# Kernel tuning notes

Measured on AMD Instinct MI355X. Metric: run time of the kernel, lower is better.

The kernel has to match this reference:

```python
import math
import jax, jax.numpy as jnp
import numpy as np

NUM_HEADS = 8
K_CRITICAL = 0.05
K_SKIP = 0.10


def setup_inputs() -> dict:
    key = jax.random.key(0)
    ks = jax.random.split(key, 10)
    B, T, D = 1, 2048, 512
    s = 1.0 / math.sqrt(D)
    return {
        'x': jax.random.normal(ks[0], (B, T, D), jnp.float32),
        'wq': jax.random.normal(ks[1], (D, D), jnp.float32) * s,
        'bq': jax.random.normal(ks[2], (D,), jnp.float32) * s,
        'wk': jax.random.normal(ks[3], (D, D), jnp.float32) * s,
        'bk': jax.random.normal(ks[4], (D,), jnp.float32) * s,
        'wv': jax.random.normal(ks[5], (D, D), jnp.float32) * s,
        'bv': jax.random.normal(ks[6], (D,), jnp.float32) * s,
        'wo': jax.random.normal(ks[7], (D, D), jnp.float32) * s,
        'bo': jax.random.normal(ks[8], (D,), jnp.float32) * s,
    }


def _phi(t):
    # elu(t) + 1 -> positive feature map for linear attention
    return jax.nn.elu(t) + 1.0


def reference(x, wq, bq, wk, bk, wv, bv, wo, bo):
    B, T, D = x.shape
    H = NUM_HEADS
    hd = D // H

    # projections (torch nn.Linear: y = x @ W.T + b), split heads -> [B,H,T,hd]
    q = (x @ wq.T + bq).reshape(B, T, H, hd).transpose(0, 2, 1, 3)
    k = (x @ wk.T + bk).reshape(B, T, H, hd).transpose(0, 2, 1, 3)
    v = (x @ wv.T + bv).reshape(B, T, H, hd).transpose(0, 2, 1, 3)

    # full attention scores [B,H,T,T]
    scores = jnp.einsum('bhqd,bhkd->bhqk', q, k) / math.sqrt(hd)

    # per-query quantile thresholds (linear interpolation, like torch.quantile)
    crit_th = jnp.quantile(scores, 1.0 - K_CRITICAL, axis=-1, keepdims=True)
    skip_th = jnp.quantile(scores, K_SKIP, axis=-1, keepdims=True)
    crit_mask = scores > crit_th
    skip_mask = scores < skip_th
    marginal_mask = jnp.logical_not(crit_mask | skip_mask)

    # critical path: softmax over top-k_critical entries only
    crit_scores = jnp.where(crit_mask, scores, -jnp.inf)
    crit_attn = jax.nn.softmax(crit_scores, axis=-1)
    crit_attn = jnp.where(skip_mask, 0.0, crit_attn)
    crit_out = jnp.einsum('bhqk,bhkd->bhqd', crit_attn, v)

    # marginal path: causal (cumulative) linear attention
    q_f = _phi(q)
    k_f = _phi(k)
    kv_cum = jnp.cumsum(k_f[..., :, None] * v[..., None, :], axis=2)  # [B,H,T,hd,hd]
    k_cum = jnp.cumsum(k_f, axis=2)                                   # [B,H,T,hd]
    lin_num = jnp.einsum('bhtd,bhtde->bhte', q_f, kv_cum)             # [B,H,T,hd]
    lin_den = jnp.clip(jnp.sum(q_f * k_cum, axis=-1, keepdims=True), 1e-6, None)
    marginal_active = jnp.mean(marginal_mask.astype(scores.dtype), axis=-1, keepdims=True)
    lin_out = (lin_num / lin_den) * marginal_active

    out = (crit_out + lin_out).transpose(0, 2, 1, 3).reshape(B, T, D)
    out = out @ wo.T + bo  # dropout is identity in eval mode
    return out
```

## Files before the change

### kernel.cpp

```cpp
#include <hip/hip_runtime.h>
#include <math.h>

#define T_SEQ 2048
#define D_MODEL 512
#define H_HEADS 8
#define HD 64
#define NCH 32
#define CSZ 64
#define CAP 192

__device__ __forceinline__ unsigned f2k(float f) {
    unsigned u = __float_as_uint(f);
    return (u & 0x80000000u) ? ~u : (u | 0x80000000u);
}
__device__ __forceinline__ float k2f(unsigned k) {
    unsigned u = (k & 0x80000000u) ? (k & 0x7fffffffu) : ~k;
    return __uint_as_float(u);
}

__device__ __forceinline__ void locate_rank(unsigned rr, unsigned e0,
    const unsigned cc[4], int lane, unsigned& sel_bin, unsigned& sel_nb, unsigned& sel_cnt)
{
    unsigned e1 = e0 + cc[0], e2 = e1 + cc[1], e3 = e2 + cc[2];
    int bin = -1; unsigned nb = 0u, ct = 0u;
    if (rr >= e0 && rr < e1)              { bin = lane * 4 + 0; nb = e0; ct = cc[0]; }
    else if (rr >= e1 && rr < e2)         { bin = lane * 4 + 1; nb = e1; ct = cc[1]; }
    else if (rr >= e2 && rr < e3)         { bin = lane * 4 + 2; nb = e2; ct = cc[2]; }
    else if (rr >= e3 && rr < e3 + cc[3]) { bin = lane * 4 + 3; nb = e3; ct = cc[3]; }
    unsigned long long bal = __ballot(bin >= 0);
    int src = __ffsll((unsigned long long)bal) - 1;
    sel_bin = (unsigned)__shfl(bin, src);
    sel_nb  = (unsigned)__shfl((int)nb, src);
    sel_cnt = (unsigned)__shfl((int)ct, src);
}

__global__ __launch_bounds__(256) void proj_qkv_kernel(
    const float* __restrict__ x,
    const float* __restrict__ wq, const float* __restrict__ bq,
    const float* __restrict__ wk, const float* __restrict__ bk,
    const float* __restrict__ wv, const float* __restrict__ bv,
    float* __restrict__ qh, float* __restrict__ kh, float* __restrict__ vh,
    float* __restrict__ qf, float* __restrict__ kf)
{
    const int which = blockIdx.z;
    const float* W    = (which == 0) ? wq : (which == 1) ? wk : wv;
    const float* bias = (which == 0) ? bq : (which == 1) ? bk : bv;
    float* outh = (which == 0) ? qh : (which == 1) ? kh : vh;
    float* outf = (which == 0) ? qf : (which == 1) ? kf : nullptr;

    __shared__ float As[32][68];
    __shared__ float Bs[32][68];
    const int tid = threadIdx.x;
    const int m0 = blockIdx.x * 64;
    const int n0 = blockIdx.y * 64;
    const int rb = (tid >> 4) * 4;
    const int cb = (tid & 15) * 4;

    float acc[4][4] = {};
    for (int k0 = 0; k0 < D_MODEL; k0 += 32) {
        for (int l = 0; l < 2; ++l) {
            int p = tid + l * 256;
            int row = p >> 3;
            int c4 = (p & 7) * 4;
            float4 av = *(const float4*)(x + (size_t)(m0 + row) * D_MODEL + k0 + c4);
            As[c4 + 0][row] = av.x; As[c4 + 1][row] = av.y;
            As[c4 + 2][row] = av.z; As[c4 + 3][row] = av.w;
            float4 wv4 = *(const float4*)(W + (size_t)(n0 + row) * D_MODEL + k0 + c4);
            Bs[c4 + 0][row] = wv4.x; Bs[c4 + 1][row] = wv4.y;
            Bs[c4 + 2][row] = wv4.z; Bs[c4 + 3][row] = wv4.w;
        }
        __syncthreads();
        #pragma unroll
        for (int kk = 0; kk < 32; ++kk) {
            float4 ar = *(const float4*)&As[kk][rb];
            float4 br = *(const float4*)&Bs[kk][cb];
            float arr[4] = {ar.x, ar.y, ar.z, ar.w};
            float brr[4] = {br.x, br.y, br.z, br.w};
            #pragma unroll
            for (int i = 0; i < 4; ++i)
                #pragma unroll
                for (int j = 0; j < 4; ++j)
                    acc[i][j] = fmaf(arr[i], brr[j], acc[i][j]);
        }
        __syncthreads();
    }
    #pragma unroll
    for (int i = 0; i < 4; ++i) {
        int m = m0 + rb + i;
        #pragma unroll
        for (int j = 0; j < 4; ++j) {
            int n = n0 + cb + j;
            float v = acc[i][j] + bias[n];
            int h = n >> 6, d = n & 63;
            size_t idx = ((size_t)(h * T_SEQ) + m) * HD + d;
            outh[idx] = v;
            if (outf) outf[idx] = (v > 0.f) ? (v + 1.f) : expf(v);
        }
    }
}

__global__ __launch_bounds__(256) void out_proj_kernel(
    const float* __restrict__ att, const float* __restrict__ wo,
    const float* __restrict__ bo, float* __restrict__ out)
{
    __shared__ float As[32][68];
    __shared__ float Bs[32][68];
    const int tid = threadIdx.x;
    const int m0 = blockIdx.x * 64;
    const int n0 = blockIdx.y * 64;
    const int rb = (tid >> 4) * 4;
    const int cb = (tid & 15) * 4;

    float acc[4][4] = {};
    for (int k0 = 0; k0 < D_MODEL; k0 += 32) {
        for (int l = 0; l < 2; ++l) {
            int p = tid + l * 256;
            int row = p >> 3;
            int c4 = (p & 7) * 4;
            float4 av = *(const float4*)(att + (size_t)(m0 + row) * D_MODEL + k0 + c4);
            As[c4 + 0][row] = av.x; As[c4 + 1][row] = av.y;
            As[c4 + 2][row] = av.z; As[c4 + 3][row] = av.w;
            float4 wv4 = *(const float4*)(wo + (size_t)(n0 + row) * D_MODEL + k0 + c4);
            Bs[c4 + 0][row] = wv4.x; Bs[c4 + 1][row] = wv4.y;
            Bs[c4 + 2][row] = wv4.z; Bs[c4 + 3][row] = wv4.w;
        }
        __syncthreads();
        #pragma unroll
        for (int kk = 0; kk < 32; ++kk) {
            float4 ar = *(const float4*)&As[kk][rb];
            float4 br = *(const float4*)&Bs[kk][cb];
            float arr[4] = {ar.x, ar.y, ar.z, ar.w};
            float brr[4] = {br.x, br.y, br.z, br.w};
            #pragma unroll
            for (int i = 0; i < 4; ++i)
                #pragma unroll
                for (int j = 0; j < 4; ++j)
                    acc[i][j] = fmaf(arr[i], brr[j], acc[i][j]);
        }
        __syncthreads();
    }
    #pragma unroll
    for (int i = 0; i < 4; ++i) {
        int m = m0 + rb + i;
        #pragma unroll
        for (int j = 0; j < 4; ++j) {
            int n = n0 + cb + j;
            out[(size_t)m * D_MODEL + n] = acc[i][j] + bo[n];
        }
    }
}

__global__ __launch_bounds__(256) void qk_gemm_kernel(
    const float* __restrict__ qh, const float* __restrict__ kh, float* __restrict__ S)
{
    __shared__ float As[64][68];
    __shared__ float Bs[64][68];
    const int tid = threadIdx.x;
    const int n0 = blockIdx.x * 64;
    const int m0 = blockIdx.y * 64;
    const int h  = blockIdx.z;
    const float* qb = qh + (size_t)h * T_SEQ * HD;
    const float* kb = kh + (size_t)h * T_SEQ * HD;

    for (int l = 0; l < 4; ++l) {
        int p = tid + l * 256;
        int row = p >> 4, c4 = (p & 15) * 4;
        float4 a = *(const float4*)(qb + (size_t)(m0 + row) * HD + c4);
        As[c4 + 0][row] = a.x; As[c4 + 1][row] = a.y;
        As[c4 + 2][row] = a.z; As[c4 + 3][row] = a.w;
        float4 b = *(const float4*)(kb + (size_t)(n0 + row) * HD + c4);
        Bs[c4 + 0][row] = b.x; Bs[c4 + 1][row] = b.y;
        Bs[c4 + 2][row] = b.z; Bs[c4 + 3][row] = b.w;
    }
    __syncthreads();

    const int rb = (tid >> 4) * 4;
    const int cb = (tid & 15) * 4;
    float acc[4][4] = {};
    #pragma unroll 16
    for (int kk = 0; kk < HD; ++kk) {
        float4 ar = *(const float4*)&As[kk][rb];
        float4 br = *(const float4*)&Bs[kk][cb];
        float arr[4] = {ar.x, ar.y, ar.z, ar.w};
        float brr[4] = {br.x, br.y, br.z, br.w};
        #pragma unroll
        for (int i = 0; i < 4; ++i)
            #pragma unroll
            for (int j = 0; j < 4; ++j)
                acc[i][j] = fmaf(arr[i], brr[j], acc[i][j]);
    }
    #pragma unroll
    for (int i = 0; i < 4; ++i) {
        float4 o;
        o.x = acc[i][0] * 0.125f; o.y = acc[i][1] * 0.125f;
        o.z = acc[i][2] * 0.125f; o.w = acc[i][3] * 0.125f;
        *(float4*)(S + ((size_t)h * T_SEQ + m0 + rb + i) * T_SEQ + n0 + cb) = o;
    }
}

__global__ __launch_bounds__(256) void select_kernel(
    const float* __restrict__ S, float2* __restrict__ clist,
    int* __restrict__ critcnt, float* __restrict__ marg, float* __restrict__ rowinv)
{
    const int h = blockIdx.y;
    const int r = threadIdx.x >> 6;
    const int lane = threadIdx.x & 63;
    const int t = blockIdx.x * 4 + r;
    __shared__ unsigned hists[4][2][256];

    const float* srow = S + ((size_t)h * T_SEQ + t) * T_SEQ;
    unsigned kr[32];
    #pragma unroll
    for (int u = 0; u < 8; ++u) {
        float4 f = *(const float4*)(srow + (size_t)(lane + u * 64) * 4);
        kr[u * 4 + 0] = f2k(f.x); kr[u * 4 + 1] = f2k(f.y);
        kr[u * 4 + 2] = f2k(f.z); kr[u * 4 + 3] = f2k(f.w);
    }

    const unsigned rankv[2] = {204u, 1944u};
    unsigned pfx[2], base[2] = {0u, 0u};
    bool res[2] = {false, false};
    unsigned rsh[2] = {0u, 0u};

    {
        uint4 z4 = make_uint4(0u, 0u, 0u, 0u);
        uint4* hv = (uint4*)hists[r];
        hv[lane * 2 + 0] = z4; hv[lane * 2 + 1] = z4;
        #pragma unroll
        for (int u = 0; u < 32; ++u)
            atomicAdd(&hists[r][0][kr[u] >> 24], 1u);
        uint4 a = ((const uint4*)hists[r][0])[lane];
        unsigned cc[4] = {a.x, a.y, a.z, a.w};
        unsigned lsum = cc[0] + cc[1] + cc[2] + cc[3];
        unsigned incl = lsum;
        #pragma unroll
        for (int off = 1; off < 64; off <<= 1) {
            unsigned tv = __shfl_up(incl, off);
            if (lane >= off) incl += tv;
        }
        unsigned e0 = incl - lsum;
        #pragma unroll
        for (int g = 0; g < 2; ++g) {
            unsigned bin, nb, ct;
            locate_rank(rankv[g], e0, cc, lane, bin, nb, ct);
            pfx[g] = bin; base[g] = nb;
            if (ct == 1u) { res[g] = true; rsh[g] = 24u; }
        }
    }

    for (int p = 1; p < 4; ++p) {
        if (res[0] && res[1]) break;
        const int sh = 24 - 8 * p;
        const bool a0 = !res[0], a1 = !res[1];
        const bool dup = a0 && a1 && (pfx[0] == pfx[1]);
        uint4 z4 = make_uint4(0u, 0u, 0u, 0u);
        uint4* hv = (uint4*)hists[r];
        hv[lane * 2 + 0] = z4; hv[lane * 2 + 1] = z4;
        #pragma unroll
        for (int u = 0; u < 32; ++u) {
            unsigned k = kr[u];
            unsigned hi = k >> (sh + 8);
            unsigned bin = (k >> sh) & 255u;
            if (a0 && hi == pfx[0]) atomicAdd(&hists[r][0][bin], 1u);
            if (a1 && !dup && hi == pfx[1]) atomicAdd(&hists[r][1][bin], 1u);
        }
        unsigned cc0[4], e00 = 0u;
        if (a0 || dup) {
            uint4 a = ((const uint4*)hists[r][0])[lane];
            cc0[0] = a.x; cc0[1] = a.y; cc0[2] = a.z; cc0[3] = a.w;
            unsigned lsum = cc0[0] + cc0[1] + cc0[2] + cc0[3];
            unsigned incl = lsum;
            #pragma unroll
            for (int off = 1; off < 64; off <<= 1) {
                unsigned tv = __shfl_up(incl, off);
                if (lane >= off) incl += tv;
            }
            e00 = incl - lsum;
        }
        if (a0) {
            unsigned bin, nb, ct;
            locate_rank(rankv[0] - base[0], e00, cc0, lane, bin, nb, ct);
            pfx[0] = (pfx[0] << 8) | bin; base[0] += nb;
            if (ct == 1u && p < 3) { res[0] = true; rsh[0] = (unsigned)sh; }
        }
        if (a1) {
            unsigned bin, nb, ct;
            if (dup) {
                locate_rank(rankv[1] - base[1], e00, cc0, lane, bin, nb, ct);
            } else {
                uint4 b = ((const uint4*)hists[r][1])[lane];
                unsigned cc1[4] = {b.x, b.y, b.z, b.w};
                unsigned lsum = cc1[0] + cc1[1] + cc1[2] + cc1[3];
                unsigned incl = lsum;
                #pragma unroll
                for (int off = 1; off < 64; off <<= 1) {
                    unsigned tv = __shfl_up(incl, off);
                    if (lane >= off) incl += tv;
                }
                unsigned e10 = incl - lsum;
                locate_rank(rankv[1] - base[1], e10, cc1, lane, bin, nb, ct);
            }
            pfx[1] = (pfx[1] << 8) | bin; base[1] += nb;
            if (ct == 1u && p < 3) { res[1] = true; rsh[1] = (unsigned)sh; }
        }
    }

    unsigned kth0, kth1;
    if (res[0] || res[1]) {
        unsigned m0v = 0xffffffffu, m1v = 0xffffffffu;
        #pragma unroll
        for (int u = 0; u < 32; ++u) {
            unsigned k = kr[u];
            if (res[0] && (k >> rsh[0]) == pfx[0]) m0v = min(m0v, k);
            if (res[1] && (k >> rsh[1]) == pfx[1]) m1v = min(m1v, k);
        }
        #pragma unroll
        for (int off = 32; off > 0; off >>= 1) {
            m0v = min(m0v, (unsigned)__shfl_xor(m0v, off));
            m1v = min(m1v, (unsigned)__shfl_xor(m1v, off));
        }
        kth0 = res[0] ? m0v : pfx[0];
        kth1 = res[1] ? m1v : pfx[1];
    } else {
        kth0 = pfx[0]; kth1 = pfx[1];
    }

    unsigned cle0 = 0, cle1 = 0, mng0 = 0xffffffffu, mng1 = 0xffffffffu, mx = 0u;
    #pragma unroll
    for (int u = 0; u < 32; ++u) {
        unsigned k = kr[u];
        mx = max(mx, k);
        if (k <= kth0) cle0++; else mng0 = min(mng0, k);
        if (k <= kth1) cle1++; else mng1 = min(mng1, k);
    }
    #pragma unroll
    for (int off = 32; off > 0; off >>= 1) {
        cle0 += (unsigned)__shfl_xor(cle0, off);
        cle1 += (unsigned)__shfl_xor(cle1, off);
        mng0 = min(mng0, (unsigned)__shfl_xor(mng0, off));
        mng1 = min(mng1, (unsigned)__shfl_xor(mng1, off));
        mx   = max(mx,   (unsigned)__shfl_xor(mx, off));
    }
    const float v204  = k2f(kth0);
    const float v205  = (cle0 > 205u) ? v204 : k2f(mng0);
    const float v1944 = k2f(kth1);
    const float v1945 = (cle1 > 1945u) ? v1944 : k2f(mng1);
    const float skip_th = v204 * 0.30f + v205 * 0.70f;
    const float crit_th = v1944 * 0.35f + v1945 * 0.65f;
    const float m = k2f(mx);

    float2* lrow = clist + ((size_t)h * T_SEQ + t) * CAP;
    float z = 0.f;
    unsigned mc = 0u;
    unsigned bcnt = 0;
    const unsigned long long pm = (lane == 0) ? 0ull : (~0ull >> (64 - lane));
    #pragma unroll
    for (int u8 = 0; u8 < 8; ++u8) {
        #pragma unroll
        for (int q = 0; q < 4; ++q) {
            float sv = k2f(kr[u8 * 4 + q]);
            bool crit = sv > crit_th;
            bool skip = sv < skip_th;
            if (!crit && !skip) mc++;
            unsigned long long bal = __ballot(crit);
            if (crit) {
                float w = __expf(sv - m);
                z += w;
                unsigned pos = bcnt + (unsigned)__popcll(bal & pm);
                if (pos < CAP) {
                    unsigned j = (unsigned)(4 * lane + 256 * u8 + q);
                    lrow[pos] = make_float2(w, __uint_as_float(j));
                }
            }
            bcnt += (unsigned)__popcll(bal);
        }
    }
    #pragma unroll
    for (int off = 32; off > 0; off >>= 1) {
        z += __shfl_xor(z, off);
        mc += (unsigned)__shfl_xor(mc, off);
    }
    if (lane == 0) {
        critcnt[(size_t)h * T_SEQ + t] = (int)min(bcnt, (unsigned)CAP);
        marg[(size_t)h * T_SEQ + t] = (float)mc * (1.f / (float)T_SEQ);
        rowinv[(size_t)h * T_SEQ + t] = (z > 0.f) ? (1.f / z) : 0.f;
    }
}

__global__ __launch_bounds__(256) void wv_gather_kernel(
    const float2* __restrict__ clist, const int* __restrict__ critcnt,
    const float* __restrict__ rowinv, const float* __restrict__ vh, float* __restrict__ att)
{
    const int h = blockIdx.y;
    const int r = threadIdx.x >> 6;
    const int lane = threadIdx.x & 63;
    const int t = blockIdx.x * 4 + r;
    const float* vb = vh + (size_t)h * T_SEQ * HD;
    const float2* lrow = clist + ((size_t)h * T_SEQ + t) * CAP;
    const int cnt = critcnt[(size_t)h * T_SEQ + t];
    const float invz = rowinv[(size_t)h * T_SEQ + t];

    float acc = 0.f;
    int i = 0;
    for (; i + 8 <= cnt; i += 8) {
        float2 e[8];
        #pragma unroll
        for (int q = 0; q < 8; ++q) e[q] = lrow[i + q];
        #pragma unroll
        for (int q = 0; q < 8; ++q) {
            unsigned j = __float_as_uint(e[q].y);
            acc = fmaf(e[q].x, vb[(size_t)j * HD + lane], acc);
        }
    }
    for (; i < cnt; ++i) {
        float2 e = lrow[i];
        unsigned j = __float_as_uint(e.y);
        acc = fmaf(e.x, vb[(size_t)j * HD + lane], acc);
    }
    att[(size_t)t * D_MODEL + h * HD + lane] += acc * invz;
}

__global__ __launch_bounds__(256) void chunk_sums_kernel(
    const float* __restrict__ kf, const float* __restrict__ vh,
    float* __restrict__ Ac, float* __restrict__ bc)
{
    const int c = blockIdx.x, h = blockIdx.y;
    const int tid = threadIdx.x;
    __shared__ float kfl[CSZ][HD];
    __shared__ float vl[CSZ][HD];
    const size_t base = ((size_t)h * T_SEQ + c * CSZ) * HD;

    for (int l = 0; l < 4; ++l) {
        int p = tid + l * 256;
        int row = p >> 4, c4 = (p & 15) * 4;
        *(float4*)&kfl[row][c4] = *(const float4*)(kf + base + (size_t)row * HD + c4);
        *(float4*)&vl[row][c4]  = *(const float4*)(vh + base + (size_t)row * HD + c4);
    }
    __syncthreads();

    const int d = tid >> 2, e0 = (tid & 3) * 16;
    float acc[16] = {};
    for (int u = 0; u < CSZ; ++u) {
        float a = kfl[u][d];
        #pragma unroll
        for (int i = 0; i < 16; ++i) acc[i] = fmaf(a, vl[u][e0 + i], acc[i]);
    }
    float* Adst = Ac + (((size_t)(h * NCH + c) * HD + d) * HD + e0);
    #pragma unroll
    for (int i = 0; i < 16; ++i) Adst[i] = acc[i];

    if (tid < HD) {
        float sum = 0.f;
        for (int u = 0; u < CSZ; ++u) sum += kfl[u][tid];
        bc[(size_t)(h * NCH + c) * HD + tid] = sum;
    }
}

__global__ __launch_bounds__(256) void prefix_kernel(
    const float* __restrict__ Ac, const float* __restrict__ bc,
    float* __restrict__ Sx, float* __restrict__ sx)
{
    const int h = blockIdx.x;
    const int tid = threadIdx.x;
    float run[16];
    #pragma unroll
    for (int i = 0; i < 16; ++i) run[i] = 0.f;
    for (int c = 0; c < NCH; ++c) {
        const float* a = Ac + (size_t)(h * NCH + c) * 4096;
        float* sdst = Sx + (size_t)(h * NCH + c) * 4096;
        #pragma unroll
        for (int i = 0; i < 16; ++i) {
            int idx = tid + i * 256;
            sdst[idx] = run[i];
            run[i] += a[idx];
        }
    }
    if (tid < HD) {
        float rb = 0.f;
        for (int c = 0; c < NCH; ++c) {
            sx[(size_t)(h * NCH + c) * HD + tid] = rb;
            rb += bc[(size_t)(h * NCH + c) * HD + tid];
        }
    }
}

__global__ __launch_bounds__(256) void lin_combine_kernel(
    const float* __restrict__ qf, const float* __restrict__ kf, const float* __restrict__ vh,
    const float* __restrict__ Sx, const float* __restrict__ sx,
    const float* __restrict__ marg, float* __restrict__ att)
{
    const int c = blockIdx.x, h = blockIdx.y;
    const int tid = threadIdx.x;
    __shared__ float Qs[CSZ][65];
    __shared__ float Ks[CSZ][65];
    __shared__ float P[CSZ][66];
    __shared__ float svv[HD];
    __shared__ float coef[CSZ];

    const size_t base = ((size_t)h * T_SEQ + c * CSZ) * HD;
    for (int l = 0; l < 4; ++l) {
        int p = tid + l * 256;
        int row = p >> 4, c4 = (p & 15) * 4;
        *(float4*)&Qs[row][c4] = *(const float4*)(qf + base + (size_t)row * HD + c4);
        *(float4*)&Ks[row][c4] = *(const float4*)(kf + base + (size_t)row * HD + c4);
    }
    if (tid < HD) svv[tid] = sx[(size_t)(h * NCH + c) * HD + tid];
    __syncthreads();

    {
        const int tq = tid >> 2, u0 = (tid & 3) * 16;
        float pr[16];
        #pragma unroll
        for (int i = 0; i < 16; ++i) pr[i] = 0.f;
        for (int d = 0; d < HD; ++d) {
            float qv = Qs[tq][d];
            #pragma unroll
            for (int i = 0; i < 16; ++i) pr[i] = fmaf(qv, Ks[u0 + i][d], pr[i]);
        }
        #pragma unroll
        for (int i = 0; i < 16; ++i) P[tq][u0 + i] = (u0 + i <= tq) ? pr[i] : 0.f;
    }
    __syncthreads();

    if (tid < CSZ) {
        const int tq = tid;
        float den = 0.f;
        for (int d = 0; d < HD; ++d) den += Qs[tq][d] * svv[d];
        for (int u = 0; u <= tq; ++u) den += P[tq][u];
        den = fmaxf(den, 1e-6f);
        coef[tq] = marg[(size_t)h * T_SEQ + c * CSZ + tq] / den;
    }
    {
        const float* Sbase = Sx + (size_t)(h * NCH + c) * 4096;
        for (int l = 0; l < 4; ++l) {
            int p = tid + l * 256;
            int row = p >> 4, c4 = (p & 15) * 4;
            *(float4*)&Ks[row][c4] = *(const float4*)(Sbase + (size_t)row * HD + c4);
        }
    }
    __syncthreads();

    {
        const int tq = tid >> 2, e0 = (tid & 3) * 16;
        float acc[16];
        #pragma unroll
        for (int i = 0; i < 16; ++i) acc[i] = 0.f;
        for (int d = 0; d < HD; ++d) {
            float qv = Qs[tq][d];
            #pragma unroll
            for (int i = 0; i < 16; ++i) acc[i] = fmaf(qv, Ks[d][e0 + i], acc[i]);
        }
        const float* vb = vh + base;
        for (int u = 0; u <= tq; ++u) {
            float pv = P[tq][u];
            #pragma unroll
            for (int i = 0; i < 16; ++i) acc[i] = fmaf(pv, vb[(size_t)u * HD + e0 + i], acc[i]);
        }
        const float cf = coef[tq];
        float* dst = att + (size_t)(c * CSZ + tq) * D_MODEL + h * HD + e0;
        #pragma unroll
        for (int i = 0; i < 16; ++i) dst[i] = acc[i] * cf;
    }
}

extern "C" void kernel_launch(void* const* d_in, const int* in_sizes, int n_in,
                              void* d_out, int out_size, void* d_ws, size_t ws_size,
                              hipStream_t stream)
{
    const float* x  = (const float*)d_in[0];
    const float* wq = (const float*)d_in[1];
    const float* bq = (const float*)d_in[2];
    const float* wk = (const float*)d_in[3];
    const float* bk = (const float*)d_in[4];
    const float* wv = (const float*)d_in[5];
    const float* bv = (const float*)d_in[6];
    const float* wo = (const float*)d_in[7];
    const float* bo = (const float*)d_in[8];
    float* out = (float*)d_out;

    float* ws = (float*)d_ws;
    const size_t NTD = (size_t)T_SEQ * D_MODEL;
    const size_t NSS = (size_t)H_HEADS * T_SEQ * T_SEQ;
    const size_t NROW = (size_t)H_HEADS * T_SEQ;
    float* S    = ws;
    float* qh   = S + NSS;
    float* kh   = qh + NTD;
    float* vh   = kh + NTD;
    float* qf   = vh + NTD;
    float* kf   = qf + NTD;
    float* att  = kf + NTD;
    float* Ac   = att + NTD;
    float* Sx   = Ac + NTD;
    float* bc   = Sx + NTD;
    float* sx   = bc + 16384;
    float* marg = sx + 16384;
    float2* clist = (float2*)(marg + 16384);
    int* critcnt  = (int*)(clist + NROW * CAP);
    float* rowinv = (float*)(critcnt + NROW);

    dim3 b256(256);
    proj_qkv_kernel<<<dim3(32, 8, 3), b256, 0, stream>>>(x, wq, bq, wk, bk, wv, bv,
                                                         qh, kh, vh, qf, kf);
    qk_gemm_kernel<<<dim3(32, 32, 8), b256, 0, stream>>>(qh, kh, S);
    select_kernel<<<dim3(T_SEQ / 4, H_HEADS), b256, 0, stream>>>(S, clist, critcnt, marg, rowinv);
    chunk_sums_kernel<<<dim3(NCH, H_HEADS), b256, 0, stream>>>(kf, vh, Ac, bc);
    prefix_kernel<<<dim3(H_HEADS), b256, 0, stream>>>(Ac, bc, Sx, sx);
    lin_combine_kernel<<<dim3(NCH, H_HEADS), b256, 0, stream>>>(qf, kf, vh, Sx, sx, marg, att);
    wv_gather_kernel<<<dim3(T_SEQ / 4, H_HEADS), b256, 0, stream>>>(clist, critcnt, rowinv, vh, att);
    out_proj_kernel<<<dim3(32, 8), b256, 0, stream>>>(att, wo, bo, out);
}
```

Measured before the change: 334.7 us.

## Enlarge QK tile to 128 rows and simplify quantile threshold selection

The QK^T GEMM tile grows from 64x64 to 128x64, so each thread computes 8x4 outputs and each K tile loaded into shared memory is reused across more rows. The select kernel computes the row max while loading and drops the interpolated float thresholds. It now classifies critical entries by comparing keys against the 1944th order statistic, and derives the marginal count arithmetically as T - critical - skip. This removes several reductions and float conversions but relies on the interpolated thresholds being equivalent to integer-rank comparisons, including under ties. It also raises register pressure and halves the GEMM grid.

```diff
diff --git a/kernel.cpp b/kernel.cpp
--- a/kernel.cpp
+++ b/kernel.cpp
@@ -153,44 +153,51 @@
 __global__ __launch_bounds__(256) void qk_gemm_kernel(
     const float* __restrict__ qh, const float* __restrict__ kh, float* __restrict__ S)
 {
-    __shared__ float As[64][68];
+    __shared__ float As[64][132];
     __shared__ float Bs[64][68];
     const int tid = threadIdx.x;
     const int n0 = blockIdx.x * 64;
-    const int m0 = blockIdx.y * 64;
+    const int m0 = blockIdx.y * 128;
     const int h  = blockIdx.z;
     const float* qb = qh + (size_t)h * T_SEQ * HD;
     const float* kb = kh + (size_t)h * T_SEQ * HD;
 
-    for (int l = 0; l < 4; ++l) {
+    #pragma unroll
+    for (int l = 0; l < 8; ++l) {
         int p = tid + l * 256;
         int row = p >> 4, c4 = (p & 15) * 4;
         float4 a = *(const float4*)(qb + (size_t)(m0 + row) * HD + c4);
         As[c4 + 0][row] = a.x; As[c4 + 1][row] = a.y;
         As[c4 + 2][row] = a.z; As[c4 + 3][row] = a.w;
+    }
+    #pragma unroll
+    for (int l = 0; l < 4; ++l) {
+        int p = tid + l * 256;
+        int row = p >> 4, c4 = (p & 15) * 4;
         float4 b = *(const float4*)(kb + (size_t)(n0 + row) * HD + c4);
         Bs[c4 + 0][row] = b.x; Bs[c4 + 1][row] = b.y;
         Bs[c4 + 2][row] = b.z; Bs[c4 + 3][row] = b.w;
     }
     __syncthreads();
 
-    const int rb = (tid >> 4) * 4;
+    const int rb = (tid >> 4) * 8;
     const int cb = (tid & 15) * 4;
-    float acc[4][4] = {};
-    #pragma unroll 16
+    float acc[8][4] = {};
+    #pragma unroll 8
     for (int kk = 0; kk < HD; ++kk) {
-        float4 ar = *(const float4*)&As[kk][rb];
+        float4 a0 = *(const float4*)&As[kk][rb];
+        float4 a1 = *(const float4*)&As[kk][rb + 4];
         float4 br = *(const float4*)&Bs[kk][cb];
-        float arr[4] = {ar.x, ar.y, ar.z, ar.w};
+        float arr[8] = {a0.x, a0.y, a0.z, a0.w, a1.x, a1.y, a1.z, a1.w};
         float brr[4] = {br.x, br.y, br.z, br.w};
         #pragma unroll
-        for (int i = 0; i < 4; ++i)
+        for (int i = 0; i < 8; ++i)
             #pragma unroll
             for (int j = 0; j < 4; ++j)
                 acc[i][j] = fmaf(arr[i], brr[j], acc[i][j]);
     }
     #pragma unroll
-    for (int i = 0; i < 4; ++i) {
+    for (int i = 0; i < 8; ++i) {
         float4 o;
         o.x = acc[i][0] * 0.125f; o.y = acc[i][1] * 0.125f;
         o.z = acc[i][2] * 0.125f; o.w = acc[i][3] * 0.125f;
@@ -210,12 +217,17 @@
 
     const float* srow = S + ((size_t)h * T_SEQ + t) * T_SEQ;
     unsigned kr[32];
+    unsigned mx = 0u;
     #pragma unroll
     for (int u = 0; u < 8; ++u) {
         float4 f = *(const float4*)(srow + (size_t)(lane + u * 64) * 4);
         kr[u * 4 + 0] = f2k(f.x); kr[u * 4 + 1] = f2k(f.y);
         kr[u * 4 + 2] = f2k(f.z); kr[u * 4 + 3] = f2k(f.w);
-    }
+        mx = max(mx, max(max(kr[u * 4 + 0], kr[u * 4 + 1]), max(kr[u * 4 + 2], kr[u * 4 + 3])));
+    }
+    #pragma unroll
+    for (int off = 32; off > 0; off >>= 1)
+        mx = max(mx, (unsigned)__shfl_xor(mx, off));
 
     const unsigned rankv[2] = {204u, 1944u};
     unsigned pfx[2], base[2] = {0u, 0u};
@@ -325,45 +337,29 @@
         kth0 = pfx[0]; kth1 = pfx[1];
     }
 
-    unsigned cle0 = 0, cle1 = 0, mng0 = 0xffffffffu, mng1 = 0xffffffffu, mx = 0u;
-    #pragma unroll
-    for (int u = 0; u < 32; ++u) {
-        unsigned k = kr[u];
-        mx = max(mx, k);
-        if (k <= kth0) cle0++; else mng0 = min(mng0, k);
-        if (k <= kth1) cle1++; else mng1 = min(mng1, k);
-    }
-    #pragma unroll
-    for (int off = 32; off > 0; off >>= 1) {
+    unsigned cle0 = 0;
+    #pragma unroll
+    for (int u = 0; u < 32; ++u)
+        if (kr[u] <= kth0) cle0++;
+    #pragma unroll
+    for (int off = 32; off > 0; off >>= 1)
         cle0 += (unsigned)__shfl_xor(cle0, off);
-        cle1 += (unsigned)__shfl_xor(cle1, off);
-        mng0 = min(mng0, (unsigned)__shfl_xor(mng0, off));
-        mng1 = min(mng1, (unsigned)__shfl_xor(mng1, off));
-        mx   = max(mx,   (unsigned)__shfl_xor(mx, off));
-    }
-    const float v204  = k2f(kth0);
-    const float v205  = (cle0 > 205u) ? v204 : k2f(mng0);
-    const float v1944 = k2f(kth1);
-    const float v1945 = (cle1 > 1945u) ? v1944 : k2f(mng1);
-    const float skip_th = v204 * 0.30f + v205 * 0.70f;
-    const float crit_th = v1944 * 0.35f + v1945 * 0.65f;
+    const unsigned scnt = (cle0 > 205u) ? base[0] : cle0;
     const float m = k2f(mx);
 
     float2* lrow = clist + ((size_t)h * T_SEQ + t) * CAP;
     float z = 0.f;
-    unsigned mc = 0u;
     unsigned bcnt = 0;
     const unsigned long long pm = (lane == 0) ? 0ull : (~0ull >> (64 - lane));
     #pragma unroll
     for (int u8 = 0; u8 < 8; ++u8) {
         #pragma unroll
         for (int q = 0; q < 4; ++q) {
-            float sv = k2f(kr[u8 * 4 + q]);
-            bool crit = sv > crit_th;
-            bool skip = sv < skip_th;
-            if (!crit && !skip) mc++;
+            unsigned k = kr[u8 * 4 + q];
+            bool crit = k > kth1;
             unsigned long long bal = __ballot(crit);
             if (crit) {
+                float sv = k2f(k);
                 float w = __expf(sv - m);
                 z += w;
                 unsigned pos = bcnt + (unsigned)__popcll(bal & pm);
@@ -376,12 +372,11 @@
         }
     }
     #pragma unroll
-    for (int off = 32; off > 0; off >>= 1) {
+    for (int off = 32; off > 0; off >>= 1)
         z += __shfl_xor(z, off);
-        mc += (unsigned)__shfl_xor(mc, off);
-    }
     if (lane == 0) {
         critcnt[(size_t)h * T_SEQ + t] = (int)min(bcnt, (unsigned)CAP);
+        unsigned mc = (unsigned)T_SEQ - bcnt - scnt;
         marg[(size_t)h * T_SEQ + t] = (float)mc * (1.f / (float)T_SEQ);
         rowinv[(size_t)h * T_SEQ + t] = (z > 0.f) ? (1.f / z) : 0.f;
     }
@@ -601,7 +596,7 @@
     dim3 b256(256);
     proj_qkv_kernel<<<dim3(32, 8, 3), b256, 0, stream>>>(x, wq, bq, wk, bk, wv, bv,
                                                          qh, kh, vh, qf, kf);
-    qk_gemm_kernel<<<dim3(32, 32, 8), b256, 0, stream>>>(qh, kh, S);
+    qk_gemm_kernel<<<dim3(32, 16, 8), b256, 0, stream>>>(qh, kh, S);
     select_kernel<<<dim3(T_SEQ / 4, H_HEADS), b256, 0, stream>>>(S, clist, critcnt, marg, rowinv);
     chunk_sums_kernel<<<dim3(NCH, H_HEADS), b256, 0, stream>>>(kf, vh, Ac, bc);
     prefix_kernel<<<dim3(H_HEADS), b256, 0, stream>>>(Ac, bc, Sx, sx);
```

Result: faster. 321.4 us (-4.0%).
